# Kernel tuning notes

Measured on AMD Instinct MI355X. Metric: run time of the kernel, lower is better.

Reference implementation:

```python
import jax, jax.numpy as jnp
import numpy as np

B, L, I, H, V, E = 48, 192, 1024, 1024, 8192, 10000
EPS = 1e-45


def setup_inputs() -> dict:
    key = jax.random.key(0)
    ks = jax.random.split(key, 16)
    s = 0.05  # scale weights so sigmoid/tanh stay in a sane range
    inp = {
        "event_table": jax.random.normal(ks[0], (E, H), jnp.float32) * s,
        "user_table": jax.random.normal(ks[1], (V, I), jnp.float32) * s,
        "start": jax.random.normal(ks[2], (1, I), jnp.float32) * s,
        "w_ih0": jax.random.normal(ks[3], (3 * H, I), jnp.float32) * s,
        "w_hh0": jax.random.normal(ks[4], (3 * H, H), jnp.float32) * s,
        "b_ih0": jax.random.normal(ks[5], (3 * H,), jnp.float32) * s,
        "b_hh0": jax.random.normal(ks[6], (3 * H,), jnp.float32) * s,
        "w_ih1": jax.random.normal(ks[7], (3 * H, H), jnp.float32) * s,
        "w_hh1": jax.random.normal(ks[8], (3 * H, H), jnp.float32) * s,
        "b_ih1": jax.random.normal(ks[9], (3 * H,), jnp.float32) * s,
        "b_hh1": jax.random.normal(ks[10], (3 * H,), jnp.float32) * s,
        "lin_w": jax.random.normal(ks[11], (V, H), jnp.float32) * s,
        "lin_b": jax.random.normal(ks[12], (V,), jnp.float32) * s,
        "ids": jax.random.randint(ks[13], (B,), 0, E, jnp.int32),
        "sequence": jax.random.randint(ks[14], (B, L), 0, V, jnp.int32),
    }
    return inp


def _gru_layer(xs, h0, w_ih, w_hh, b_ih, b_hh):
    # xs: [T, B, in]; h0: [B, H]. PyTorch GRU gate order: r, z, n.
    xp = jnp.einsum('tbi,gi->tbg', xs, w_ih) + b_ih  # [T, B, 3H]

    def step(h, xp_t):
        hp = h @ w_hh.T + b_hh                       # [B, 3H]
        xr, xz, xn = jnp.split(xp_t, 3, axis=-1)
        hr, hz, hn = jnp.split(hp, 3, axis=-1)
        r = jax.nn.sigmoid(xr + hr)
        z = jax.nn.sigmoid(xz + hz)
        n = jnp.tanh(xn + r * hn)
        h_new = (1.0 - z) * n + z * h
        return h_new, h_new

    _, ys = jax.lax.scan(step, h0, xp)
    return ys  # [T, B, H]


def reference(event_table, user_table, start, w_ih0, w_hh0, b_ih0, b_hh0,
              w_ih1, w_hh1, b_ih1, b_hh1, lin_w, lin_b, ids, sequence):
    # hx = embedding(ids, event); same initial state for every layer
    h0 = event_table[ids]                            # [B, H]
    # x = [start; user embeddings of sequence] along time: [L+1, B, I]
    xs = jnp.concatenate(
        [jnp.broadcast_to(start[None, :, :], (1, sequence.shape[0], start.shape[-1])),
         jnp.transpose(user_table[sequence], (1, 0, 2))], axis=0)
    ys = _gru_layer(xs, h0, w_ih0, w_hh0, b_ih0, b_hh0)
    ys = _gru_layer(ys, h0, w_ih1, w_hh1, b_ih1, b_hh1)
    logits = jnp.einsum('tbh,vh->btv', ys, lin_w) + lin_b  # [B, T, V]

    # SequenceMaskedSoftmax: for step i (< L-1), mask keeps ids in seq[:, i:].
    # Vectorized: suffix-max of one-hot over the sequence axis.
    onehot = jax.nn.one_hot(sequence, V, dtype=logits.dtype)      # [B, L, V]
    suffix = jax.lax.cummax(onehot, axis=1, reverse=True)          # [B, L, V]
    masked = logits.at[:, :L - 1, :].add(jnp.log(suffix[:, :L - 1, :] + EPS))
    return jax.nn.softmax(masked, axis=-1)
```

## Files before the change

kernel.cpp:

```cpp
#include <hip/hip_runtime.h>
#include <cstddef>
#include <cstdint>

constexpr int B  = 48;
constexpr int L  = 192;
constexpr int T  = 193;
constexpr int KD = 1024;
constexpr int G3 = 3072;
constexpr int V  = 8192;
constexpr int M  = T * B;
constexpr int SB = 128;

typedef float f32x4 __attribute__((ext_vector_type(4)));
typedef short s16x8 __attribute__((ext_vector_type(8)));
typedef unsigned short u16x8 __attribute__((ext_vector_type(8)));

__device__ inline unsigned short f2bf(float f) {
  unsigned u = __builtin_bit_cast(unsigned, f);
  u += 0x7fffu + ((u >> 16) & 1u);
  return (unsigned short)(u >> 16);
}
__device__ inline float bf2f(unsigned short h) {
  return __builtin_bit_cast(float, (unsigned)h << 16);
}

__global__ __launch_bounds__(256)
void init_h0(const float* __restrict__ et, const int* __restrict__ ids,
             float* __restrict__ h0f, unsigned short* __restrict__ h0hi,
             unsigned short* __restrict__ h0lo) {
  int b = blockIdx.x;
  int id = ids[b];
  float4 v = ((const float4*)(et + (size_t)id * KD))[threadIdx.x];
  ((float4*)(h0f + (size_t)b * KD))[threadIdx.x] = v;
  int base = b * KD + threadIdx.x * 4;
  float vv[4] = {v.x, v.y, v.z, v.w};
#pragma unroll
  for (int j = 0; j < 4; ++j) {
    unsigned short hi = f2bf(vv[j]);
    h0hi[base + j] = hi;
    h0lo[base + j] = f2bf(vv[j] - bf2f(hi));
  }
}

__global__ __launch_bounds__(256)
void cvt_bf16(const float* __restrict__ in, unsigned short* __restrict__ out,
              long long n) {
  long long i = ((long long)blockIdx.x * 256 + threadIdx.x) * 8;
  if (i + 8 > n) return;
  float4 v0 = *(const float4*)(in + i);
  float4 v1 = *(const float4*)(in + i + 4);
  u16x8 o;
  o[0] = f2bf(v0.x); o[1] = f2bf(v0.y); o[2] = f2bf(v0.z); o[3] = f2bf(v0.w);
  o[4] = f2bf(v1.x); o[5] = f2bf(v1.y); o[6] = f2bf(v1.z); o[7] = f2bf(v1.w);
  *(u16x8*)(out + i) = o;
}

__global__ __launch_bounds__(256)
void repack_whh(const float* __restrict__ w_hh, unsigned short* __restrict__ hi,
                unsigned short* __restrict__ lo) {
  long long idx = ((long long)blockIdx.x * 256 + threadIdx.x) * 8;
  if (idx >= (long long)SB * 32 * KD) return;
  int k  = (int)(idx & (KD - 1));
  int rr = (int)(idx >> 10);
  int r = rr & 31, bid = rr >> 5;
  u16x8 h8 = (u16x8)0, l8 = (u16x8)0;
  if (r < 24) {
    int g = r >> 3, c = bid * 8 + (r & 7);
    const float* src = w_hh + ((size_t)(g * KD + c)) * KD + k;
    float4 v0 = *(const float4*)src, v1 = *(const float4*)(src + 4);
    float vv[8] = {v0.x, v0.y, v0.z, v0.w, v1.x, v1.y, v1.z, v1.w};
#pragma unroll
    for (int j = 0; j < 8; ++j) {
      unsigned short h = f2bf(vv[j]);
      h8[j] = h;
      l8[j] = f2bf(vv[j] - bf2f(h));
    }
  }
  *(u16x8*)(hi + idx) = h8;
  *(u16x8*)(lo + idx) = l8;
}

__global__ __launch_bounds__(256)
void repack_w_single(const float* __restrict__ w, unsigned short* __restrict__ pk) {
  long long idx = ((long long)blockIdx.x * 256 + threadIdx.x) * 8;
  if (idx >= (long long)SB * 32 * KD) return;
  int k  = (int)(idx & (KD - 1));
  int rr = (int)(idx >> 10);
  int r = rr & 31, bid = rr >> 5;
  u16x8 h8 = (u16x8)0;
  if (r < 24) {
    int g = r >> 3, c = bid * 8 + (r & 7);
    const float* src = w + ((size_t)(g * KD + c)) * KD + k;
    float4 v0 = *(const float4*)src, v1 = *(const float4*)(src + 4);
    float vv[8] = {v0.x, v0.y, v0.z, v0.w, v1.x, v1.y, v1.z, v1.w};
#pragma unroll
    for (int j = 0; j < 8; ++j) h8[j] = f2bf(vv[j]);
  }
  *(u16x8*)(pk + idx) = h8;
}

template<int GATHER, int OUTMODE>
__global__ __launch_bounds__(256)
void gemm_bf16(const unsigned short* __restrict__ A,
               const unsigned short* __restrict__ W,
               const float* __restrict__ bias, float* __restrict__ C, int Ndim,
               const int* __restrict__ seq,
               const unsigned short* __restrict__ start_bf,
               const unsigned short* __restrict__ table_bf) {
  __shared__ __align__(16) unsigned short a_s[128 * 32];
  __shared__ __align__(16) unsigned short b_s[128 * 32];
  const int tid  = threadIdx.x;
  const int lane = tid & 63;
  const int wave = tid >> 6;
  const int m0 = blockIdx.x * 128;
  const int n0 = blockIdx.y * 128;
  const int wr = wave >> 1, wc = wave & 1;

  f32x4 acc[4][4];
#pragma unroll
  for (int i = 0; i < 4; ++i)
#pragma unroll
    for (int j = 0; j < 4; ++j) acc[i][j] = (f32x4){0.f, 0.f, 0.f, 0.f};

  const int lrow = lane & 15;
  const int lkhi = lane >> 4;

  for (int kt = 0; kt < KD; kt += 32) {
    __syncthreads();
#pragma unroll
    for (int j = 0; j < 2; ++j) {
      int flat = tid * 16 + j * 4096;
      int row = flat >> 6;
      int cc = (flat >> 4) & 3;
      const unsigned short* src;
      if (GATHER) {
        int m = m0 + row; if (m >= M) m = 0;
        int t = m / B, b = m - t * B;
        const unsigned short* rowsrc =
            (t == 0) ? start_bf : (table_bf + (size_t)seq[b * L + t - 1] * KD);
        src = rowsrc + kt + cc * 8;
      } else {
        int m = m0 + row; if (m >= M) m = 0;
        src = A + (size_t)m * KD + kt + cc * 8;
      }
      *(int4*)((char*)a_s + flat) = *(const int4*)src;
    }
#pragma unroll
    for (int j = 0; j < 2; ++j) {
      int flat = tid * 16 + j * 4096;
      int row = flat >> 6;
      int cc = (flat >> 4) & 3;
      const unsigned short* src = W + (size_t)(n0 + row) * KD + kt + cc * 8;
      *(int4*)((char*)b_s + flat) = *(const int4*)src;
    }
    __syncthreads();

    s16x8 af[4], wf[4];
#pragma unroll
    for (int i = 0; i < 4; ++i) {
      int arow = wr * 64 + i * 16 + lrow;
      af[i] = *(const s16x8*)((const char*)a_s + arow * 64 + lkhi * 16);
      int brow = wc * 64 + i * 16 + lrow;
      wf[i] = *(const s16x8*)((const char*)b_s + brow * 64 + lkhi * 16);
    }
#pragma unroll
    for (int i = 0; i < 4; ++i)
#pragma unroll
      for (int j = 0; j < 4; ++j)
        acc[i][j] = __builtin_amdgcn_mfma_f32_16x16x32_bf16(af[i], wf[j],
                                                            acc[i][j], 0, 0, 0);
  }

#pragma unroll
  for (int i = 0; i < 4; ++i) {
#pragma unroll
    for (int r = 0; r < 4; ++r) {
      int m = m0 + wr * 64 + i * 16 + (lane >> 4) * 4 + r;
      if (m >= M) continue;
      size_t rowoff;
      if (OUTMODE == 0) {
        rowoff = (size_t)m * (size_t)Ndim;
      } else {
        int t = m / B, b = m - t * B;
        rowoff = ((size_t)b * T + t) * (size_t)Ndim;
      }
#pragma unroll
      for (int j = 0; j < 4; ++j) {
        int n = n0 + wc * 64 + j * 16 + (lane & 15);
        C[rowoff + n] = acc[i][j][r] + bias[n];
      }
    }
  }
}

template<int HASX>
__device__ __forceinline__ void gru_core(
    int c0, int tid,
    const float* __restrict__ xp_t, const unsigned short* __restrict__ Xhi,
    const unsigned short* __restrict__ wih_pk, const float* __restrict__ b_ih,
    const unsigned short* __restrict__ wb_hi, const unsigned short* __restrict__ wb_lo,
    const float* __restrict__ b_hh,
    const unsigned short* __restrict__ Shi, const unsigned short* __restrict__ Slo,
    const float* __restrict__ h_old, float* __restrict__ h_new,
    unsigned short* __restrict__ y_hi, unsigned short* __restrict__ y_lo,
    float (*cp_h)[48 * 33], float (*cp_x)[48 * 33]) {
  const int lane = tid & 63, wave = tid >> 6;
  const int lrow = lane & 15, lkhi = lane >> 4;

  f32x4 acc_h[3][2], acc_x[3][2];
#pragma unroll
  for (int i = 0; i < 3; ++i)
#pragma unroll
    for (int j = 0; j < 2; ++j) {
      acc_h[i][j] = (f32x4){0.f, 0.f, 0.f, 0.f};
      acc_x[i][j] = (f32x4){0.f, 0.f, 0.f, 0.f};
    }

#pragma unroll
  for (int ks = 0; ks < 8; ++ks) {
    int k0 = wave * 256 + ks * 32 + lkhi * 8;
    s16x8 ah[3], al[3], xh[3];
#pragma unroll
    for (int mt = 0; mt < 3; ++mt) {
      int b = mt * 16 + lrow;
      ah[mt] = *(const s16x8*)(Shi + (size_t)b * KD + k0);
      al[mt] = *(const s16x8*)(Slo + (size_t)b * KD + k0);
      if (HASX) xh[mt] = *(const s16x8*)(Xhi + (size_t)b * KD + k0);
    }
    s16x8 bh[2], bl[2], wx[2];
#pragma unroll
    for (int nt = 0; nt < 2; ++nt) {
      int r = nt * 16 + lrow;
      bh[nt] = *(const s16x8*)(wb_hi + (size_t)r * KD + k0);
      bl[nt] = *(const s16x8*)(wb_lo + (size_t)r * KD + k0);
      if (HASX) wx[nt] = *(const s16x8*)(wih_pk + (size_t)r * KD + k0);
    }
#pragma unroll
    for (int mt = 0; mt < 3; ++mt)
#pragma unroll
      for (int nt = 0; nt < 2; ++nt) {
        acc_h[mt][nt] = __builtin_amdgcn_mfma_f32_16x16x32_bf16(ah[mt], bh[nt], acc_h[mt][nt], 0, 0, 0);
        acc_h[mt][nt] = __builtin_amdgcn_mfma_f32_16x16x32_bf16(al[mt], bh[nt], acc_h[mt][nt], 0, 0, 0);
        acc_h[mt][nt] = __builtin_amdgcn_mfma_f32_16x16x32_bf16(ah[mt], bl[nt], acc_h[mt][nt], 0, 0, 0);
        if (HASX)
          acc_x[mt][nt] = __builtin_amdgcn_mfma_f32_16x16x32_bf16(xh[mt], wx[nt], acc_x[mt][nt], 0, 0, 0);
      }
  }

#pragma unroll
  for (int mt = 0; mt < 3; ++mt)
#pragma unroll
    for (int nt = 0; nt < 2; ++nt)
#pragma unroll
      for (int r = 0; r < 4; ++r) {
        int row = mt * 16 + (lane >> 4) * 4 + r;
        int col = nt * 16 + (lane & 15);
        cp_h[wave][row * 33 + col] = acc_h[mt][nt][r];
        if (HASX) cp_x[wave][row * 33 + col] = acc_x[mt][nt][r];
      }
  __syncthreads();

  for (int p = tid; p < 384; p += 256) {
    int b = p >> 3, c = p & 7;
    float pr = 0.f, pz = 0.f, pn = 0.f;
    float xr, xz, xn;
#pragma unroll
    for (int w = 0; w < 4; ++w) {
      pr += cp_h[w][b * 33 + c];
      pz += cp_h[w][b * 33 + 8 + c];
      pn += cp_h[w][b * 33 + 16 + c];
    }
    int gc = c0 + c;
    if (HASX) {
      float qr = 0.f, qz = 0.f, qn = 0.f;
#pragma unroll
      for (int w = 0; w < 4; ++w) {
        qr += cp_x[w][b * 33 + c];
        qz += cp_x[w][b * 33 + 8 + c];
        qn += cp_x[w][b * 33 + 16 + c];
      }
      xr = qr + b_ih[gc];
      xz = qz + b_ih[KD + gc];
      xn = qn + b_ih[2 * KD + gc];
    } else {
      const float* xrow = xp_t + (size_t)b * G3;
      xr = xrow[gc]; xz = xrow[KD + gc]; xn = xrow[2 * KD + gc];
    }
    float hr = pr + b_hh[gc];
    float hz = pz + b_hh[KD + gc];
    float hn = pn + b_hh[2 * KD + gc];
    float r_ = 1.f / (1.f + expf(-(xr + hr)));
    float z_ = 1.f / (1.f + expf(-(xz + hz)));
    float n_ = tanhf(xn + r_ * hn);
    float hold = h_old[(size_t)b * KD + gc];
    float hnew = (1.f - z_) * n_ + z_ * hold;
    h_new[(size_t)b * KD + gc] = hnew;
    unsigned short hi = f2bf(hnew);
    y_hi[(size_t)b * KD + gc] = hi;
    y_lo[(size_t)b * KD + gc] = f2bf(hnew - bf2f(hi));
  }
}

__global__ __launch_bounds__(256)
void gru_pipe(int t,
              const float* __restrict__ xp0,
              const unsigned short* __restrict__ wpk0_hi,
              const unsigned short* __restrict__ wpk0_lo,
              const float* __restrict__ b_hh0,
              const unsigned short* __restrict__ wpk1_hi,
              const unsigned short* __restrict__ wpk1_lo,
              const unsigned short* __restrict__ wih1pk,
              const float* __restrict__ b_ih1,
              const float* __restrict__ b_hh1,
              const unsigned short* __restrict__ h0hi,
              const unsigned short* __restrict__ h0lo,
              const float* __restrict__ h0f,
              unsigned short* __restrict__ ys0_bf,
              unsigned short* __restrict__ lo0a, unsigned short* __restrict__ lo0b,
              float* __restrict__ h0f32,
              unsigned short* __restrict__ ys1_bf,
              unsigned short* __restrict__ lo1a, unsigned short* __restrict__ lo1b,
              float* __restrict__ h1f32) {
  __shared__ float cp_h[4][48 * 33];
  __shared__ float cp_x[4][48 * 33];
  const int tid = threadIdx.x;
  const bool is1 = blockIdx.x >= SB;
  const int bid = is1 ? (int)blockIdx.x - SB : (int)blockIdx.x;
  const int c0 = bid * 8;

  if (!is1) {
    if (t >= T) return;
    const unsigned short* Shi = (t == 0) ? h0hi : ys0_bf + (size_t)(t - 1) * B * KD;
    const unsigned short* Slo = (t == 0) ? h0lo : (((t - 1) & 1) ? lo0b : lo0a);
    const float* hold = (t == 0) ? h0f : h0f32;
    gru_core<0>(c0, tid, xp0 + (size_t)t * B * G3, nullptr, nullptr, nullptr,
                wpk0_hi + (size_t)bid * 32 * KD, wpk0_lo + (size_t)bid * 32 * KD,
                b_hh0, Shi, Slo, hold, h0f32,
                ys0_bf + (size_t)t * B * KD, (t & 1) ? lo0b : lo0a,
                cp_h, cp_x);
  } else {
    int s = t - 1;
    if (s < 0) return;
    const unsigned short* Shi = (s == 0) ? h0hi : ys1_bf + (size_t)(s - 1) * B * KD;
    const unsigned short* Slo = (s == 0) ? h0lo : (((s - 1) & 1) ? lo1b : lo1a);
    const float* hold = (s == 0) ? h0f : h1f32;
    gru_core<1>(c0, tid, nullptr, ys0_bf + (size_t)s * B * KD,
                wih1pk + (size_t)bid * 32 * KD, b_ih1,
                wpk1_hi + (size_t)bid * 32 * KD, wpk1_lo + (size_t)bid * 32 * KD,
                b_hh1, Shi, Slo, hold, h1f32,
                ys1_bf + (size_t)s * B * KD, (s & 1) ? lo1b : lo1a,
                cp_h, cp_x);
  }
}

__global__ __launch_bounds__(256)
void softmax_mask(float* __restrict__ out, const int* __restrict__ seq) {
  const int t = blockIdx.x, b = blockIdx.y;
  float* row = out + ((size_t)b * T + t) * V;
  __shared__ unsigned bits[V / 32];
  __shared__ float red[4];
  const int tid = threadIdx.x;
  const bool masked = (t < L - 1);
  if (masked) {
    bits[tid] = 0u;
    __syncthreads();
    int rem = L - t;
    if (tid < rem) {
      int id = seq[b * L + t + tid];
      atomicOr(&bits[id >> 5], 1u << (id & 31));
    }
  }
  __syncthreads();

  float4 x[8];
  float mx = -3.0e38f;
#pragma unroll
  for (int j = 0; j < 8; ++j) {
    float4 v = ((const float4*)row)[j * 256 + tid];
    if (masked) {
      int vb = (j * 256 + tid) * 4;
      unsigned wrd = bits[vb >> 5];
      int sh = vb & 31;
      if (!((wrd >> (sh + 0)) & 1u)) v.x = -1.0e30f;
      if (!((wrd >> (sh + 1)) & 1u)) v.y = -1.0e30f;
      if (!((wrd >> (sh + 2)) & 1u)) v.z = -1.0e30f;
      if (!((wrd >> (sh + 3)) & 1u)) v.w = -1.0e30f;
    }
    x[j] = v;
    mx = fmaxf(mx, fmaxf(fmaxf(v.x, v.y), fmaxf(v.z, v.w)));
  }
#pragma unroll
  for (int off = 32; off > 0; off >>= 1) mx = fmaxf(mx, __shfl_xor(mx, off));
  int wv = tid >> 6;
  if ((tid & 63) == 0) red[wv] = mx;
  __syncthreads();
  mx = fmaxf(fmaxf(red[0], red[1]), fmaxf(red[2], red[3]));

  float s = 0.f;
#pragma unroll
  for (int j = 0; j < 8; ++j) {
    x[j].x = expf(x[j].x - mx); x[j].y = expf(x[j].y - mx);
    x[j].z = expf(x[j].z - mx); x[j].w = expf(x[j].w - mx);
    s += x[j].x + x[j].y + x[j].z + x[j].w;
  }
#pragma unroll
  for (int off = 32; off > 0; off >>= 1) s += __shfl_xor(s, off);
  __syncthreads();
  if ((tid & 63) == 0) red[wv] = s;
  __syncthreads();
  s = red[0] + red[1] + red[2] + red[3];
  float inv = 1.f / s;
#pragma unroll
  for (int j = 0; j < 8; ++j) {
    float4 v = make_float4(x[j].x * inv, x[j].y * inv, x[j].z * inv, x[j].w * inv);
    ((float4*)row)[j * 256 + tid] = v;
  }
}

extern "C" void kernel_launch(void* const* d_in, const int* in_sizes, int n_in,
                              void* d_out, int out_size, void* d_ws, size_t ws_size,
                              hipStream_t stream) {
  const float* event_table = (const float*)d_in[0];
  const float* user_table  = (const float*)d_in[1];
  const float* startv      = (const float*)d_in[2];
  const float* w_ih0 = (const float*)d_in[3];
  const float* w_hh0 = (const float*)d_in[4];
  const float* b_ih0 = (const float*)d_in[5];
  const float* b_hh0 = (const float*)d_in[6];
  const float* w_ih1 = (const float*)d_in[7];
  const float* w_hh1 = (const float*)d_in[8];
  const float* b_ih1 = (const float*)d_in[9];
  const float* b_hh1 = (const float*)d_in[10];
  const float* lin_w = (const float*)d_in[11];
  const float* lin_b = (const float*)d_in[12];
  const int*   ids   = (const int*)d_in[13];
  const int*   seq   = (const int*)d_in[14];
  float* out = (float*)d_out;

  float* xp0  = (float*)d_ws;
  float* h0f  = xp0 + (size_t)M * G3;
  float* h0f32 = h0f + (size_t)B * KD;
  float* h1f32 = h0f32 + (size_t)B * KD;
  unsigned short* ut_bf    = (unsigned short*)(h1f32 + (size_t)B * KD);
  unsigned short* start_bf = ut_bf    + (size_t)V * KD;
  unsigned short* wih0_bf  = start_bf + KD;
  unsigned short* linw_bf  = wih0_bf  + (size_t)G3 * KD;
  unsigned short* ys0_bf   = linw_bf  + (size_t)V * KD;
  unsigned short* ys1_bf   = ys0_bf   + (size_t)M * KD;
  unsigned short* h0hi     = ys1_bf   + (size_t)M * KD;
  unsigned short* h0lo     = h0hi + (size_t)B * KD;
  unsigned short* lo0a     = h0lo + (size_t)B * KD;
  unsigned short* lo0b     = lo0a + (size_t)B * KD;
  unsigned short* lo1a     = lo0b + (size_t)B * KD;
  unsigned short* lo1b     = lo1a + (size_t)B * KD;
  unsigned short* wpk0_hi  = lo1b + (size_t)B * KD;
  unsigned short* wpk0_lo  = wpk0_hi + (size_t)SB * 32 * KD;
  unsigned short* wpk1_hi  = wpk0_lo + (size_t)SB * 32 * KD;
  unsigned short* wpk1_lo  = wpk1_hi + (size_t)SB * 32 * KD;
  unsigned short* wih1pk   = wpk1_lo + (size_t)SB * 32 * KD;

  init_h0<<<dim3(B), 256, 0, stream>>>(event_table, ids, h0f, h0hi, h0lo);

  auto cvt = [&](const float* src, unsigned short* dst, long long n) {
    int blocks = (int)((n + 2047) / 2048);
    cvt_bf16<<<dim3(blocks), 256, 0, stream>>>(src, dst, n);
  };
  cvt(user_table, ut_bf,    (long long)V * KD);
  cvt(startv,     start_bf, KD);
  cvt(w_ih0,      wih0_bf,  (long long)G3 * KD);
  cvt(lin_w,      linw_bf,  (long long)V * KD);

  repack_whh<<<dim3(SB * 32 * KD / 2048), 256, 0, stream>>>(w_hh0, wpk0_hi, wpk0_lo);
  repack_whh<<<dim3(SB * 32 * KD / 2048), 256, 0, stream>>>(w_hh1, wpk1_hi, wpk1_lo);
  repack_w_single<<<dim3(SB * 32 * KD / 2048), 256, 0, stream>>>(w_ih1, wih1pk);

  gemm_bf16<1, 0><<<dim3((M + 127) / 128, G3 / 128), 256, 0, stream>>>(
      nullptr, wih0_bf, b_ih0, xp0, G3, seq, start_bf, ut_bf);

  for (int t = 0; t <= T; ++t) {
    gru_pipe<<<dim3(2 * SB), 256, 0, stream>>>(
        t, xp0, wpk0_hi, wpk0_lo, b_hh0, wpk1_hi, wpk1_lo, wih1pk, b_ih1, b_hh1,
        h0hi, h0lo, h0f, ys0_bf, lo0a, lo0b, h0f32, ys1_bf, lo1a, lo1b, h1f32);
  }

  gemm_bf16<0, 1><<<dim3((M + 127) / 128, V / 128), 256, 0, stream>>>(
      ys1_bf, linw_bf, lin_b, out, V, nullptr, nullptr, nullptr);

  softmax_mask<<<dim3(T, B), 256, 0, stream>>>(out, seq);
}
```

Baseline: 4.076 ms.

## Replace per-step GRU kernel launches with a persistent kernel and grid barrier

The 194 per-timestep launches of the pipelined two-layer GRU kernel are replaced by one persistent kernel of 256 blocks that loops over time and synchronises with an atomic grid barrier. This removes per-launch overhead and the launch gap between recurrent steps. It relies on all 256 blocks being co-resident, which is not guaranteed. The barrier also has a spin timeout that silently breaks out, so there is a correctness risk if blocks are delayed.

```diff
diff --git a/kernel.cpp b/kernel.cpp
--- a/kernel.cpp
+++ b/kernel.cpp
@@ -301,26 +301,40 @@
   }
 }
 
-__global__ __launch_bounds__(256)
-void gru_pipe(int t,
-              const float* __restrict__ xp0,
-              const unsigned short* __restrict__ wpk0_hi,
-              const unsigned short* __restrict__ wpk0_lo,
-              const float* __restrict__ b_hh0,
-              const unsigned short* __restrict__ wpk1_hi,
-              const unsigned short* __restrict__ wpk1_lo,
-              const unsigned short* __restrict__ wih1pk,
-              const float* __restrict__ b_ih1,
-              const float* __restrict__ b_hh1,
-              const unsigned short* __restrict__ h0hi,
-              const unsigned short* __restrict__ h0lo,
-              const float* __restrict__ h0f,
-              unsigned short* __restrict__ ys0_bf,
-              unsigned short* __restrict__ lo0a, unsigned short* __restrict__ lo0b,
-              float* __restrict__ h0f32,
-              unsigned short* __restrict__ ys1_bf,
-              unsigned short* __restrict__ lo1a, unsigned short* __restrict__ lo1b,
-              float* __restrict__ h1f32) {
+__device__ __forceinline__ void grid_barrier(unsigned* bar) {
+  __syncthreads();
+  if (threadIdx.x == 0) {
+    __threadfence();
+    unsigned g = __atomic_load_n(bar + 1, __ATOMIC_RELAXED);
+    unsigned arrived = __atomic_add_fetch(bar, 1u, __ATOMIC_ACQ_REL);
+    if (arrived == 2u * SB) {
+      __atomic_store_n(bar, 0u, __ATOMIC_RELAXED);
+      __atomic_store_n(bar + 1, g + 1u, __ATOMIC_RELEASE);
+    } else {
+      int spins = 0;
+      while (__atomic_load_n(bar + 1, __ATOMIC_ACQUIRE) == g) {
+        if (++spins > (1 << 18)) break;
+        __builtin_amdgcn_s_sleep(2);
+      }
+    }
+    __threadfence();
+  }
+  __syncthreads();
+}
+
+struct ScanArgs {
+  const float* xp0;
+  const unsigned short* wpk0_hi; const unsigned short* wpk0_lo; const float* b_hh0;
+  const unsigned short* wpk1_hi; const unsigned short* wpk1_lo;
+  const unsigned short* wih1pk;  const float* b_ih1; const float* b_hh1;
+  const unsigned short* h0hi;    const unsigned short* h0lo; const float* h0f;
+  unsigned short* ys0_bf; unsigned short* lo0a; unsigned short* lo0b; float* h0f32;
+  unsigned short* ys1_bf; unsigned short* lo1a; unsigned short* lo1b; float* h1f32;
+  unsigned* bar;
+};
+
+__global__ __launch_bounds__(256, 1)
+void gru_scan_persist(ScanArgs a) {
   __shared__ float cp_h[4][48 * 33];
   __shared__ float cp_x[4][48 * 33];
   const int tid = threadIdx.x;
@@ -328,28 +342,33 @@
   const int bid = is1 ? (int)blockIdx.x - SB : (int)blockIdx.x;
   const int c0 = bid * 8;
 
-  if (!is1) {
-    if (t >= T) return;
-    const unsigned short* Shi = (t == 0) ? h0hi : ys0_bf + (size_t)(t - 1) * B * KD;
-    const unsigned short* Slo = (t == 0) ? h0lo : (((t - 1) & 1) ? lo0b : lo0a);
-    const float* hold = (t == 0) ? h0f : h0f32;
-    gru_core<0>(c0, tid, xp0 + (size_t)t * B * G3, nullptr, nullptr, nullptr,
-                wpk0_hi + (size_t)bid * 32 * KD, wpk0_lo + (size_t)bid * 32 * KD,
-                b_hh0, Shi, Slo, hold, h0f32,
-                ys0_bf + (size_t)t * B * KD, (t & 1) ? lo0b : lo0a,
-                cp_h, cp_x);
-  } else {
-    int s = t - 1;
-    if (s < 0) return;
-    const unsigned short* Shi = (s == 0) ? h0hi : ys1_bf + (size_t)(s - 1) * B * KD;
-    const unsigned short* Slo = (s == 0) ? h0lo : (((s - 1) & 1) ? lo1b : lo1a);
-    const float* hold = (s == 0) ? h0f : h1f32;
-    gru_core<1>(c0, tid, nullptr, ys0_bf + (size_t)s * B * KD,
-                wih1pk + (size_t)bid * 32 * KD, b_ih1,
-                wpk1_hi + (size_t)bid * 32 * KD, wpk1_lo + (size_t)bid * 32 * KD,
-                b_hh1, Shi, Slo, hold, h1f32,
-                ys1_bf + (size_t)s * B * KD, (s & 1) ? lo1b : lo1a,
-                cp_h, cp_x);
+  for (int t = 0; t <= T; ++t) {
+    if (!is1) {
+      if (t < T) {
+        const unsigned short* Shi = (t == 0) ? a.h0hi : a.ys0_bf + (size_t)(t - 1) * B * KD;
+        const unsigned short* Slo = (t == 0) ? a.h0lo : (((t - 1) & 1) ? a.lo0b : a.lo0a);
+        const float* hold = (t == 0) ? a.h0f : a.h0f32;
+        gru_core<0>(c0, tid, a.xp0 + (size_t)t * B * G3, nullptr, nullptr, nullptr,
+                    a.wpk0_hi + (size_t)bid * 32 * KD, a.wpk0_lo + (size_t)bid * 32 * KD,
+                    a.b_hh0, Shi, Slo, hold, a.h0f32,
+                    a.ys0_bf + (size_t)t * B * KD, (t & 1) ? a.lo0b : a.lo0a,
+                    cp_h, cp_x);
+      }
+    } else {
+      int s = t - 1;
+      if (s >= 0) {
+        const unsigned short* Shi = (s == 0) ? a.h0hi : a.ys1_bf + (size_t)(s - 1) * B * KD;
+        const unsigned short* Slo = (s == 0) ? a.h0lo : (((s - 1) & 1) ? a.lo1b : a.lo1a);
+        const float* hold = (s == 0) ? a.h0f : a.h1f32;
+        gru_core<1>(c0, tid, nullptr, a.ys0_bf + (size_t)s * B * KD,
+                    a.wih1pk + (size_t)bid * 32 * KD, a.b_ih1,
+                    a.wpk1_hi + (size_t)bid * 32 * KD, a.wpk1_lo + (size_t)bid * 32 * KD,
+                    a.b_hh1, Shi, Slo, hold, a.h1f32,
+                    a.ys1_bf + (size_t)s * B * KD, (s & 1) ? a.lo1b : a.lo1a,
+                    cp_h, cp_x);
+      }
+    }
+    grid_barrier(a.bar);
   }
 }
 
@@ -458,6 +477,7 @@
   unsigned short* wpk1_hi  = wpk0_lo + (size_t)SB * 32 * KD;
   unsigned short* wpk1_lo  = wpk1_hi + (size_t)SB * 32 * KD;
   unsigned short* wih1pk   = wpk1_lo + (size_t)SB * 32 * KD;
+  unsigned* bar            = (unsigned*)(wih1pk + (size_t)SB * 32 * KD);
 
   init_h0<<<dim3(B), 256, 0, stream>>>(event_table, ids, h0f, h0hi, h0lo);
 
@@ -477,10 +497,18 @@
   gemm_bf16<1, 0><<<dim3((M + 127) / 128, G3 / 128), 256, 0, stream>>>(
       nullptr, wih0_bf, b_ih0, xp0, G3, seq, start_bf, ut_bf);
 
-  for (int t = 0; t <= T; ++t) {
-    gru_pipe<<<dim3(2 * SB), 256, 0, stream>>>(
-        t, xp0, wpk0_hi, wpk0_lo, b_hh0, wpk1_hi, wpk1_lo, wih1pk, b_ih1, b_hh1,
-        h0hi, h0lo, h0f, ys0_bf, lo0a, lo0b, h0f32, ys1_bf, lo1a, lo1b, h1f32);
+  hipMemsetAsync(bar, 0, 2 * sizeof(unsigned), stream);
+  {
+    ScanArgs sa;
+    sa.xp0 = xp0;
+    sa.wpk0_hi = wpk0_hi; sa.wpk0_lo = wpk0_lo; sa.b_hh0 = b_hh0;
+    sa.wpk1_hi = wpk1_hi; sa.wpk1_lo = wpk1_lo;
+    sa.wih1pk = wih1pk;   sa.b_ih1 = b_ih1;     sa.b_hh1 = b_hh1;
+    sa.h0hi = h0hi; sa.h0lo = h0lo; sa.h0f = h0f;
+    sa.ys0_bf = ys0_bf; sa.lo0a = lo0a; sa.lo0b = lo0b; sa.h0f32 = h0f32;
+    sa.ys1_bf = ys1_bf; sa.lo1a = lo1a; sa.lo1b = lo1b; sa.h1f32 = h1f32;
+    sa.bar = bar;
+    gru_scan_persist<<<dim3(2 * SB), dim3(256), 0, stream>>>(sa);
   }
 
   gemm_bf16<0, 1><<<dim3((M + 127) / 128, V / 128), 256, 0, stream>>>(
```

Measured after the change: 13.00 ms. +219.0%, slower.
